# Optimization experiments

Hardware: AMD Instinct MI355X
Metric: run time of the kernel (lower is better)

Reference implementation:

```python
import jax, jax.numpy as jnp
import numpy as np

NUM_STEPS = 8
SLOPE = 25.0        # snntorch surrogate.fast_sigmoid default slope
MAX_STD = 2.0
MIN_STD = 0.1
STATE_DIM = 6
HIDDEN = 128
OUT = 1
BATCH = 65536
W_STD = 0.01


@jax.custom_vjp
def spike(x):
    # heaviside(x) with fast-sigmoid surrogate gradient
    return (x > 0).astype(x.dtype)

def _spike_fwd(x):
    return spike(x), x

def _spike_bwd(x, g):
    return (g / (SLOPE * jnp.abs(x) + 1.0) ** 2,)

spike.defvjp(_spike_fwd, _spike_bwd)


def setup_inputs() -> dict:
    key = jax.random.key(0)
    ks = jax.random.split(key, 8)
    state = jax.random.normal(ks[0], (BATCH, STATE_DIM), dtype=jnp.float32)
    w_fc1 = W_STD * jax.random.normal(ks[1], (HIDDEN, STATE_DIM), dtype=jnp.float32)
    w_rec1 = W_STD * jax.random.normal(ks[2], (HIDDEN, HIDDEN), dtype=jnp.float32)
    w_fc2 = W_STD * jax.random.normal(ks[3], (HIDDEN, HIDDEN), dtype=jnp.float32)
    w_rec2 = W_STD * jax.random.normal(ks[4], (HIDDEN, HIDDEN), dtype=jnp.float32)
    w_mean = W_STD * jax.random.normal(ks[5], (OUT, HIDDEN), dtype=jnp.float32)
    w_std = W_STD * jax.random.normal(ks[6], (OUT, HIDDEN), dtype=jnp.float32)
    return {
        "state": state,
        "w_fc1": w_fc1, "w_rec1": w_rec1,
        "w_fc2": w_fc2, "w_rec2": w_rec2,
        "w_mean": w_mean, "w_std": w_std,
        "alpha1": jnp.float32(0.9), "beta1": jnp.float32(0.9), "thr1": jnp.float32(1.0),
        "alpha2": jnp.float32(0.9), "beta2": jnp.float32(0.9), "thr2": jnp.float32(1.0),
    }


def _snn_forward(state, w_fc1, w_rec1, w_fc2, w_rec2, w_mean, w_std,
                 alpha1, beta1, thr1, alpha2, beta2, thr2):
    a1 = jnp.clip(alpha1, 0.0, 1.0); b1 = jnp.clip(beta1, 0.0, 1.0)
    a2 = jnp.clip(alpha2, 0.0, 1.0); b2 = jnp.clip(beta2, 0.0, 1.0)

    B = state.shape[0]
    cur1_in = state @ w_fc1.T  # constant across steps: [B, H]
    z = jnp.zeros((B, HIDDEN), dtype=state.dtype)

    def step(carry, _):
        syn1, mem1, spk1, syn2, mem2, spk2 = carry
        # layer 1: snntorch Synaptic (reset-by-subtract, reset from prev mem, detached)
        reset1 = jax.lax.stop_gradient((mem1 - thr1 > 0).astype(mem1.dtype))
        syn1 = a1 * syn1 + cur1_in + spk1 @ w_rec1.T
        mem1 = b1 * mem1 + syn1 - reset1 * thr1
        spk1 = spike(mem1 - thr1)
        # layer 2
        reset2 = jax.lax.stop_gradient((mem2 - thr2 > 0).astype(mem2.dtype))
        syn2 = a2 * syn2 + spk1 @ w_fc2.T + spk2 @ w_rec2.T
        mem2 = b2 * mem2 + syn2 - reset2 * thr2
        spk2 = spike(mem2 - thr2)
        return (syn1, mem1, spk1, syn2, mem2, spk2), spk2

    init = (z, z, z, z, z, z)
    _, spk_rec = jax.lax.scan(step, init, None, length=NUM_STEPS)  # [T, B, H]
    avg_spikes = spk_rec.mean(axis=0)  # [B, H]

    value_mean = jnp.tanh(avg_spikes @ w_mean.T)
    value_std = (MAX_STD - MIN_STD) * jax.nn.sigmoid(avg_spikes @ w_std.T + 2.0) + MIN_STD
    return value_mean, value_std


def reference(state, w_fc1, w_rec1, w_fc2, w_rec2, w_mean, w_std,
              alpha1, beta1, thr1, alpha2, beta2, thr2):
    return _snn_forward(state, w_fc1, w_rec1, w_fc2, w_rec2, w_mean, w_std,
                        alpha1, beta1, thr1, alpha2, beta2, thr2)
```

## Files before the change

kernel.cpp:

```cpp
#include <hip/hip_runtime.h>
#include <cmath>


typedef float f32x2 __attribute__((ext_vector_type(2)));
typedef float f32x4 __attribute__((ext_vector_type(4)));

constexpr int BATCH = 65536;
constexpr int HID   = 128;
constexpr int SDIM  = 6;
constexpr int NSTEP = 8;
constexpr int BLOCK = 1024;
constexpr int GRID  = 256;
constexpr int WAVES_TOTAL = GRID * (BLOCK / 64);
constexpr int ELEMS_PER_WAVE = BATCH / WAVES_TOTAL;
constexpr int PAIRS = ELEMS_PER_WAVE / 2;

__global__ __launch_bounds__(BLOCK) void snn_fwd(
    const float* __restrict__ state,
    const float* __restrict__ w_fc1,
    const float* __restrict__ w_rec1,
    const float* __restrict__ w_fc2,
    const float* __restrict__ w_rec2,
    const float* __restrict__ w_mean,
    const float* __restrict__ w_std,
    const float* __restrict__ p_alpha1, const float* __restrict__ p_beta1,
    const float* __restrict__ p_thr1,
    const float* __restrict__ p_alpha2, const float* __restrict__ p_beta2,
    const float* __restrict__ p_thr2,
    float* __restrict__ out)
{
    __shared__ f32x4 ldw[HID * 64];

    const int tid = threadIdx.x;

    for (int v = tid; v < HID * 64; v += BLOCK) {
        const int l = v >> 7;
        const int j = v & 127;
        const int pos = (j << 6) | (l ^ (j & 63));
        f32x4 w;
        w.x = w_rec1[l * HID + j];
        w.y = w_rec1[(l + 64) * HID + j];
        w.z = w_fc2 [l * HID + j];
        w.w = w_fc2 [(l + 64) * HID + j];
        ldw[pos] = w;
    }

    const int lane  = tid & 63;
    const int gwave = blockIdx.x * (BLOCK / 64) + (tid >> 6);

    f32x2 w1[SDIM];
    #pragma unroll
    for (int k = 0; k < SDIM; ++k) {
        w1[k].x = w_fc1[lane * SDIM + k];
        w1[k].y = w_fc1[(lane + 64) * SDIM + k];
    }
    const float wm_a = w_mean[lane], wm_b = w_mean[lane + 64];
    const float ws_a = w_std [lane], ws_b = w_std [lane + 64];

    const float a1 = fminf(fmaxf(p_alpha1[0], 0.f), 1.f);
    const float b1 = fminf(fmaxf(p_beta1 [0], 0.f), 1.f);
    const float a2 = fminf(fmaxf(p_alpha2[0], 0.f), 1.f);
    const float b2 = fminf(fmaxf(p_beta2 [0], 0.f), 1.f);
    const float t1 = p_thr1[0];
    const float t2 = p_thr2[0];
    const f32x2 a1v = {a1, a1}, b1v = {b1, b1}, a2v = {a2, a2}, b2v = {b2, b2};

    const float* __restrict__ rec2_a = w_rec2 + lane * HID;
    const float* __restrict__ rec2_b = w_rec2 + (lane + 64) * HID;

    __syncthreads();

    auto walk2 = [&](unsigned long long m, const f32x4* __restrict__ base,
                     f32x2& f, f32x2& r) {
        if (!m) return;
        int j = __builtin_ctzll(m); m &= m - 1;
        f32x4 w = base[(j << 6) | (lane ^ j)];
        while (m) {
            const int j2 = __builtin_ctzll(m); m &= m - 1;
            const f32x4 w2 = base[(j2 << 6) | (lane ^ j2)];
            r += __builtin_shufflevector(w, w, 0, 1);
            f += __builtin_shufflevector(w, w, 2, 3);
            w = w2;
        }
        r += __builtin_shufflevector(w, w, 0, 1);
        f += __builtin_shufflevector(w, w, 2, 3);
    };
    auto walkg = [&](unsigned long long m, int jbase, f32x2& f) {
        while (m) {
            const int j = __builtin_ctzll(m) + jbase; m &= m - 1;
            f.x += rec2_a[j];
            f.y += rec2_b[j];
        }
    };

    const f32x4* __restrict__ baseLo = ldw;
    const f32x4* __restrict__ baseHi = ldw + (64 << 6);

    float sx[SDIM], sy[SDIM];
    #pragma unroll
    for (int k = 0; k < SDIM; ++k) {
        sx[k] = state[(gwave) * SDIM + k];
        sy[k] = state[(gwave + WAVES_TOTAL) * SDIM + k];
    }

    for (int e = 0; e < PAIRS; ++e) {
        const int bx = gwave + WAVES_TOTAL * (2 * e);
        const int by = gwave + WAVES_TOTAL * (2 * e + 1);

        f32x2 curx = {0.f, 0.f}, cury = {0.f, 0.f};
        #pragma unroll
        for (int k = 0; k < SDIM; ++k) {
            const f32x2 sxv = {sx[k], sx[k]};
            const f32x2 syv = {sy[k], sy[k]};
            curx = __builtin_elementwise_fma(sxv, w1[k], curx);
            cury = __builtin_elementwise_fma(syv, w1[k], cury);
        }

        float sxn[SDIM], syn2p[SDIM];
        if (e + 1 < PAIRS) {
            const int bxn = gwave + WAVES_TOTAL * (2 * e + 2);
            const int byn = gwave + WAVES_TOTAL * (2 * e + 3);
            #pragma unroll
            for (int k = 0; k < SDIM; ++k) {
                sxn[k]   = state[bxn * SDIM + k];
                syn2p[k] = state[byn * SDIM + k];
            }
        }

        f32x2 s1x = {0.f, 0.f}, m1x = {0.f, 0.f}, s2x = {0.f, 0.f}, m2x = {0.f, 0.f};
        f32x2 s1y = {0.f, 0.f}, m1y = {0.f, 0.f}, s2y = {0.f, 0.f}, m2y = {0.f, 0.f};
        bool k1xa = false, k1xb = false, k2xa = false, k2xb = false;
        bool k1ya = false, k1yb = false, k2ya = false, k2yb = false;
        f32x2 cx = {0.f, 0.f}, cy = {0.f, 0.f};
        unsigned long long M2xa = 0ull, M2xb = 0ull, M2ya = 0ull, M2yb = 0ull;
        f32x2 rx = {0.f, 0.f}, ry = {0.f, 0.f};

        #pragma unroll 1
        for (int t = 0; t < NSTEP; ++t) {
            s1x = __builtin_elementwise_fma(a1v, s1x, curx + rx);
            s1y = __builtin_elementwise_fma(a1v, s1y, cury + ry);
            const f32x2 rst1x = {k1xa ? t1 : 0.f, k1xb ? t1 : 0.f};
            const f32x2 rst1y = {k1ya ? t1 : 0.f, k1yb ? t1 : 0.f};
            m1x = __builtin_elementwise_fma(b1v, m1x, s1x) - rst1x;
            m1y = __builtin_elementwise_fma(b1v, m1y, s1y) - rst1y;
            k1xa = (m1x.x - t1) > 0.f;
            k1xb = (m1x.y - t1) > 0.f;
            k1ya = (m1y.x - t1) > 0.f;
            k1yb = (m1y.y - t1) > 0.f;
            const unsigned long long M1xa = __ballot(k1xa);
            const unsigned long long M1xb = __ballot(k1xb);
            const unsigned long long M1ya = __ballot(k1ya);
            const unsigned long long M1yb = __ballot(k1yb);

            f32x2 fx = {0.f, 0.f}, fy = {0.f, 0.f};
            rx = (f32x2){0.f, 0.f}; ry = (f32x2){0.f, 0.f};
            walk2(M1xa, baseLo, fx, rx);
            walk2(M1ya, baseLo, fy, ry);
            walk2(M1xb, baseHi, fx, rx);
            walk2(M1yb, baseHi, fy, ry);

            if ((M2xa | M2xb | M2ya | M2yb) != 0ull) {
                walkg(M2xa, 0,  fx);
                walkg(M2xb, 64, fx);
                walkg(M2ya, 0,  fy);
                walkg(M2yb, 64, fy);
            }

            s2x = __builtin_elementwise_fma(a2v, s2x, fx);
            s2y = __builtin_elementwise_fma(a2v, s2y, fy);
            const f32x2 rst2x = {k2xa ? t2 : 0.f, k2xb ? t2 : 0.f};
            const f32x2 rst2y = {k2ya ? t2 : 0.f, k2yb ? t2 : 0.f};
            m2x = __builtin_elementwise_fma(b2v, m2x, s2x) - rst2x;
            m2y = __builtin_elementwise_fma(b2v, m2y, s2y) - rst2y;
            k2xa = (m2x.x - t2) > 0.f;
            k2xb = (m2x.y - t2) > 0.f;
            k2ya = (m2y.x - t2) > 0.f;
            k2yb = (m2y.y - t2) > 0.f;
            M2xa = __ballot(k2xa);
            M2xb = __ballot(k2xb);
            M2ya = __ballot(k2ya);
            M2yb = __ballot(k2yb);
            const f32x2 onex = {k2xa ? 1.f : 0.f, k2xb ? 1.f : 0.f};
            const f32x2 oney = {k2ya ? 1.f : 0.f, k2yb ? 1.f : 0.f};
            cx += onex;
            cy += oney;
        }

        const float axa = cx.x * (1.f / (float)NSTEP);
        const float axb = cx.y * (1.f / (float)NSTEP);
        const float aya = cy.x * (1.f / (float)NSTEP);
        const float ayb = cy.y * (1.f / (float)NSTEP);
        float dmx = axa * wm_a + axb * wm_b;
        float dsx = axa * ws_a + axb * ws_b;
        float dmy = aya * wm_a + ayb * wm_b;
        float dsy = aya * ws_a + ayb * ws_b;
        #pragma unroll
        for (int off = 32; off > 0; off >>= 1) {
            dmx += __shfl_xor(dmx, off, 64);
            dsx += __shfl_xor(dsx, off, 64);
            dmy += __shfl_xor(dmy, off, 64);
            dsy += __shfl_xor(dsy, off, 64);
        }
        if (lane == 0) {
            out[bx] = tanhf(dmx);
            out[by] = tanhf(dmy);
            const float sgx = 1.f / (1.f + expf(-(dsx + 2.f)));
            const float sgy = 1.f / (1.f + expf(-(dsy + 2.f)));
            out[BATCH + bx] = 1.9f * sgx + 0.1f;
            out[BATCH + by] = 1.9f * sgy + 0.1f;
        }

        if (e + 1 < PAIRS) {
            #pragma unroll
            for (int k = 0; k < SDIM; ++k) { sx[k] = sxn[k]; sy[k] = syn2p[k]; }
        }
    }
}

extern "C" void kernel_launch(void* const* d_in, const int* in_sizes, int n_in,
                              void* d_out, int out_size, void* d_ws, size_t ws_size,
                              hipStream_t stream) {
    (void)in_sizes; (void)n_in; (void)d_ws; (void)ws_size; (void)out_size;
    snn_fwd<<<GRID, BLOCK, 0, stream>>>(
        (const float*)d_in[0],
        (const float*)d_in[1],
        (const float*)d_in[2],
        (const float*)d_in[3],
        (const float*)d_in[4],
        (const float*)d_in[5],
        (const float*)d_in[6],
        (const float*)d_in[7],
        (const float*)d_in[8],
        (const float*)d_in[9],
        (const float*)d_in[10],
        (const float*)d_in[11],
        (const float*)d_in[12],
        (float*)d_out);
}
```

Measured before the change: 122.4 us.

## Pack recurrent weights into global workspace and read via cache instead of LDS

Adds a small pre-pass kernel that packs w_rec1 and w_fc2 into an interleaved f32x4 layout in the workspace buffer. The main kernel then reads that layout straight from global memory (L1/L2) instead of staging 128 KB into shared memory per block. This removes the per-block LDS fill and barrier and lifts the LDS occupancy limit, allowing smaller 512-thread blocks with more waves per CU. The cost is an extra kernel launch and gathers served by cache rather than LDS, which may have higher latency. The original LDS kernel is kept as a fallback when no workspace is available.

```diff
diff --git a/kernel.cpp b/kernel.cpp
--- a/kernel.cpp
+++ b/kernel.cpp
@@ -9,17 +9,33 @@
 constexpr int HID   = 128;
 constexpr int SDIM  = 6;
 constexpr int NSTEP = 8;
-constexpr int BLOCK = 1024;
-constexpr int GRID  = 256;
-constexpr int WAVES_TOTAL = GRID * (BLOCK / 64);
-constexpr int ELEMS_PER_WAVE = BATCH / WAVES_TOTAL;
-constexpr int PAIRS = ELEMS_PER_WAVE / 2;
-
-__global__ __launch_bounds__(BLOCK) void snn_fwd(
+
+__global__ __launch_bounds__(256) void pack_weights(
+    const float* __restrict__ w_rec1,
+    const float* __restrict__ w_fc2,
+    f32x4* __restrict__ P)
+{
+    const int g = blockIdx.x * 256 + threadIdx.x;
+    const int j = g & 127;
+    const int l = g >> 7;
+    f32x4 w;
+    w.x = w_rec1[l * HID + j];
+    w.y = w_rec1[(l + 64) * HID + j];
+    w.z = w_fc2 [l * HID + j];
+    w.w = w_fc2 [(l + 64) * HID + j];
+    P[(j << 6) | l] = w;
+}
+
+constexpr int BLOCK_G = 512;
+constexpr int GRID_G  = 1024;
+constexpr int WAVES_G = GRID_G * (BLOCK_G / 64);
+constexpr int EPW_G   = BATCH / WAVES_G;
+constexpr int PAIRS_G = EPW_G / 2;
+
+__global__ __launch_bounds__(BLOCK_G, 8) void snn_fwd_g(
     const float* __restrict__ state,
     const float* __restrict__ w_fc1,
-    const float* __restrict__ w_rec1,
-    const float* __restrict__ w_fc2,
+    const f32x4* __restrict__ P,
     const float* __restrict__ w_rec2,
     const float* __restrict__ w_mean,
     const float* __restrict__ w_std,
@@ -29,24 +45,9 @@
     const float* __restrict__ p_thr2,
     float* __restrict__ out)
 {
-    __shared__ f32x4 ldw[HID * 64];
-
-    const int tid = threadIdx.x;
-
-    for (int v = tid; v < HID * 64; v += BLOCK) {
-        const int l = v >> 7;
-        const int j = v & 127;
-        const int pos = (j << 6) | (l ^ (j & 63));
-        f32x4 w;
-        w.x = w_rec1[l * HID + j];
-        w.y = w_rec1[(l + 64) * HID + j];
-        w.z = w_fc2 [l * HID + j];
-        w.w = w_fc2 [(l + 64) * HID + j];
-        ldw[pos] = w;
-    }
-
+    const int tid   = threadIdx.x;
     const int lane  = tid & 63;
-    const int gwave = blockIdx.x * (BLOCK / 64) + (tid >> 6);
+    const int gwave = blockIdx.x * (BLOCK_G / 64) + (tid >> 6);
 
     f32x2 w1[SDIM];
     #pragma unroll
@@ -68,16 +69,17 @@
     const float* __restrict__ rec2_a = w_rec2 + lane * HID;
     const float* __restrict__ rec2_b = w_rec2 + (lane + 64) * HID;
 
-    __syncthreads();
+    const f32x4* __restrict__ baseLo = P;
+    const f32x4* __restrict__ baseHi = P + (64 << 6);
 
     auto walk2 = [&](unsigned long long m, const f32x4* __restrict__ base,
                      f32x2& f, f32x2& r) {
         if (!m) return;
         int j = __builtin_ctzll(m); m &= m - 1;
-        f32x4 w = base[(j << 6) | (lane ^ j)];
+        f32x4 w = base[(j << 6) | lane];
         while (m) {
             const int j2 = __builtin_ctzll(m); m &= m - 1;
-            const f32x4 w2 = base[(j2 << 6) | (lane ^ j2)];
+            const f32x4 w2 = base[(j2 << 6) | lane];
             r += __builtin_shufflevector(w, w, 0, 1);
             f += __builtin_shufflevector(w, w, 2, 3);
             w = w2;
@@ -93,19 +95,16 @@
         }
     };
 
-    const f32x4* __restrict__ baseLo = ldw;
-    const f32x4* __restrict__ baseHi = ldw + (64 << 6);
-
     float sx[SDIM], sy[SDIM];
     #pragma unroll
     for (int k = 0; k < SDIM; ++k) {
         sx[k] = state[(gwave) * SDIM + k];
-        sy[k] = state[(gwave + WAVES_TOTAL) * SDIM + k];
-    }
-
-    for (int e = 0; e < PAIRS; ++e) {
-        const int bx = gwave + WAVES_TOTAL * (2 * e);
-        const int by = gwave + WAVES_TOTAL * (2 * e + 1);
+        sy[k] = state[(gwave + WAVES_G) * SDIM + k];
+    }
+
+    for (int e = 0; e < PAIRS_G; ++e) {
+        const int bx = gwave + WAVES_G * (2 * e);
+        const int by = gwave + WAVES_G * (2 * e + 1);
 
         f32x2 curx = {0.f, 0.f}, cury = {0.f, 0.f};
         #pragma unroll
@@ -117,9 +116,9 @@
         }
 
         float sxn[SDIM], syn2p[SDIM];
-        if (e + 1 < PAIRS) {
-            const int bxn = gwave + WAVES_TOTAL * (2 * e + 2);
-            const int byn = gwave + WAVES_TOTAL * (2 * e + 3);
+        if (e + 1 < PAIRS_G) {
+            const int bxn = gwave + WAVES_G * (2 * e + 2);
+            const int byn = gwave + WAVES_G * (2 * e + 3);
             #pragma unroll
             for (int k = 0; k < SDIM; ++k) {
                 sxn[k]   = state[bxn * SDIM + k];
@@ -210,7 +209,214 @@
             out[BATCH + by] = 1.9f * sgy + 0.1f;
         }
 
-        if (e + 1 < PAIRS) {
+        if (e + 1 < PAIRS_G) {
+            #pragma unroll
+            for (int k = 0; k < SDIM; ++k) { sx[k] = sxn[k]; sy[k] = syn2p[k]; }
+        }
+    }
+}
+
+constexpr int BLOCK_L = 1024;
+constexpr int GRID_L  = 256;
+constexpr int WAVES_L = GRID_L * (BLOCK_L / 64);
+constexpr int EPW_L   = BATCH / WAVES_L;
+constexpr int PAIRS_L = EPW_L / 2;
+
+__global__ __launch_bounds__(BLOCK_L) void snn_fwd_lds(
+    const float* __restrict__ state,
+    const float* __restrict__ w_fc1,
+    const float* __restrict__ w_rec1,
+    const float* __restrict__ w_fc2,
+    const float* __restrict__ w_rec2,
+    const float* __restrict__ w_mean,
+    const float* __restrict__ w_std,
+    const float* __restrict__ p_alpha1, const float* __restrict__ p_beta1,
+    const float* __restrict__ p_thr1,
+    const float* __restrict__ p_alpha2, const float* __restrict__ p_beta2,
+    const float* __restrict__ p_thr2,
+    float* __restrict__ out)
+{
+    __shared__ f32x4 ldw[HID * 64];
+    const int tid = threadIdx.x;
+
+    for (int v = tid; v < HID * 64; v += BLOCK_L) {
+        const int l = v >> 7;
+        const int j = v & 127;
+        const int pos = (j << 6) | (l ^ (j & 63));
+        f32x4 w;
+        w.x = w_rec1[l * HID + j];
+        w.y = w_rec1[(l + 64) * HID + j];
+        w.z = w_fc2 [l * HID + j];
+        w.w = w_fc2 [(l + 64) * HID + j];
+        ldw[pos] = w;
+    }
+
+    const int lane  = tid & 63;
+    const int gwave = blockIdx.x * (BLOCK_L / 64) + (tid >> 6);
+
+    f32x2 w1[SDIM];
+    #pragma unroll
+    for (int k = 0; k < SDIM; ++k) {
+        w1[k].x = w_fc1[lane * SDIM + k];
+        w1[k].y = w_fc1[(lane + 64) * SDIM + k];
+    }
+    const float wm_a = w_mean[lane], wm_b = w_mean[lane + 64];
+    const float ws_a = w_std [lane], ws_b = w_std [lane + 64];
+
+    const float a1 = fminf(fmaxf(p_alpha1[0], 0.f), 1.f);
+    const float b1 = fminf(fmaxf(p_beta1 [0], 0.f), 1.f);
+    const float a2 = fminf(fmaxf(p_alpha2[0], 0.f), 1.f);
+    const float b2 = fminf(fmaxf(p_beta2 [0], 0.f), 1.f);
+    const float t1 = p_thr1[0];
+    const float t2 = p_thr2[0];
+    const f32x2 a1v = {a1, a1}, b1v = {b1, b1}, a2v = {a2, a2}, b2v = {b2, b2};
+
+    const float* __restrict__ rec2_a = w_rec2 + lane * HID;
+    const float* __restrict__ rec2_b = w_rec2 + (lane + 64) * HID;
+
+    __syncthreads();
+
+    auto walk2 = [&](unsigned long long m, const f32x4* __restrict__ base,
+                     f32x2& f, f32x2& r) {
+        if (!m) return;
+        int j = __builtin_ctzll(m); m &= m - 1;
+        f32x4 w = base[(j << 6) | (lane ^ j)];
+        while (m) {
+            const int j2 = __builtin_ctzll(m); m &= m - 1;
+            const f32x4 w2 = base[(j2 << 6) | (lane ^ j2)];
+            r += __builtin_shufflevector(w, w, 0, 1);
+            f += __builtin_shufflevector(w, w, 2, 3);
+            w = w2;
+        }
+        r += __builtin_shufflevector(w, w, 0, 1);
+        f += __builtin_shufflevector(w, w, 2, 3);
+    };
+    auto walkg = [&](unsigned long long m, int jbase, f32x2& f) {
+        while (m) {
+            const int j = __builtin_ctzll(m) + jbase; m &= m - 1;
+            f.x += rec2_a[j];
+            f.y += rec2_b[j];
+        }
+    };
+
+    const f32x4* __restrict__ baseLo = ldw;
+    const f32x4* __restrict__ baseHi = ldw + (64 << 6);
+
+    float sx[SDIM], sy[SDIM];
+    #pragma unroll
+    for (int k = 0; k < SDIM; ++k) {
+        sx[k] = state[(gwave) * SDIM + k];
+        sy[k] = state[(gwave + WAVES_L) * SDIM + k];
+    }
+
+    for (int e = 0; e < PAIRS_L; ++e) {
+        const int bx = gwave + WAVES_L * (2 * e);
+        const int by = gwave + WAVES_L * (2 * e + 1);
+
+        f32x2 curx = {0.f, 0.f}, cury = {0.f, 0.f};
+        #pragma unroll
+        for (int k = 0; k < SDIM; ++k) {
+            const f32x2 sxv = {sx[k], sx[k]};
+            const f32x2 syv = {sy[k], sy[k]};
+            curx = __builtin_elementwise_fma(sxv, w1[k], curx);
+            cury = __builtin_elementwise_fma(syv, w1[k], cury);
+        }
+
+        float sxn[SDIM], syn2p[SDIM];
+        if (e + 1 < PAIRS_L) {
+            const int bxn = gwave + WAVES_L * (2 * e + 2);
+            const int byn = gwave + WAVES_L * (2 * e + 3);
+            #pragma unroll
+            for (int k = 0; k < SDIM; ++k) {
+                sxn[k]   = state[bxn * SDIM + k];
+                syn2p[k] = state[byn * SDIM + k];
+            }
+        }
+
+        f32x2 s1x = {0.f, 0.f}, m1x = {0.f, 0.f}, s2x = {0.f, 0.f}, m2x = {0.f, 0.f};
+        f32x2 s1y = {0.f, 0.f}, m1y = {0.f, 0.f}, s2y = {0.f, 0.f}, m2y = {0.f, 0.f};
+        bool k1xa = false, k1xb = false, k2xa = false, k2xb = false;
+        bool k1ya = false, k1yb = false, k2ya = false, k2yb = false;
+        f32x2 cx = {0.f, 0.f}, cy = {0.f, 0.f};
+        unsigned long long M2xa = 0ull, M2xb = 0ull, M2ya = 0ull, M2yb = 0ull;
+        f32x2 rx = {0.f, 0.f}, ry = {0.f, 0.f};
+
+        #pragma unroll 1
+        for (int t = 0; t < NSTEP; ++t) {
+            s1x = __builtin_elementwise_fma(a1v, s1x, curx + rx);
+            s1y = __builtin_elementwise_fma(a1v, s1y, cury + ry);
+            const f32x2 rst1x = {k1xa ? t1 : 0.f, k1xb ? t1 : 0.f};
+            const f32x2 rst1y = {k1ya ? t1 : 0.f, k1yb ? t1 : 0.f};
+            m1x = __builtin_elementwise_fma(b1v, m1x, s1x) - rst1x;
+            m1y = __builtin_elementwise_fma(b1v, m1y, s1y) - rst1y;
+            k1xa = (m1x.x - t1) > 0.f;
+            k1xb = (m1x.y - t1) > 0.f;
+            k1ya = (m1y.x - t1) > 0.f;
+            k1yb = (m1y.y - t1) > 0.f;
+            const unsigned long long M1xa = __ballot(k1xa);
+            const unsigned long long M1xb = __ballot(k1xb);
+            const unsigned long long M1ya = __ballot(k1ya);
+            const unsigned long long M1yb = __ballot(k1yb);
+
+            f32x2 fx = {0.f, 0.f}, fy = {0.f, 0.f};
+            rx = (f32x2){0.f, 0.f}; ry = (f32x2){0.f, 0.f};
+            walk2(M1xa, baseLo, fx, rx);
+            walk2(M1ya, baseLo, fy, ry);
+            walk2(M1xb, baseHi, fx, rx);
+            walk2(M1yb, baseHi, fy, ry);
+
+            if ((M2xa | M2xb | M2ya | M2yb) != 0ull) {
+                walkg(M2xa, 0,  fx);
+                walkg(M2xb, 64, fx);
+                walkg(M2ya, 0,  fy);
+                walkg(M2yb, 64, fy);
+            }
+
+            s2x = __builtin_elementwise_fma(a2v, s2x, fx);
+            s2y = __builtin_elementwise_fma(a2v, s2y, fy);
+            const f32x2 rst2x = {k2xa ? t2 : 0.f, k2xb ? t2 : 0.f};
+            const f32x2 rst2y = {k2ya ? t2 : 0.f, k2yb ? t2 : 0.f};
+            m2x = __builtin_elementwise_fma(b2v, m2x, s2x) - rst2x;
+            m2y = __builtin_elementwise_fma(b2v, m2y, s2y) - rst2y;
+            k2xa = (m2x.x - t2) > 0.f;
+            k2xb = (m2x.y - t2) > 0.f;
+            k2ya = (m2y.x - t2) > 0.f;
+            k2yb = (m2y.y - t2) > 0.f;
+            M2xa = __ballot(k2xa);
+            M2xb = __ballot(k2xb);
+            M2ya = __ballot(k2ya);
+            M2yb = __ballot(k2yb);
+            const f32x2 onex = {k2xa ? 1.f : 0.f, k2xb ? 1.f : 0.f};
+            const f32x2 oney = {k2ya ? 1.f : 0.f, k2yb ? 1.f : 0.f};
+            cx += onex;
+            cy += oney;
+        }
+
+        const float axa = cx.x * (1.f / (float)NSTEP);
+        const float axb = cx.y * (1.f / (float)NSTEP);
+        const float aya = cy.x * (1.f / (float)NSTEP);
+        const float ayb = cy.y * (1.f / (float)NSTEP);
+        float dmx = axa * wm_a + axb * wm_b;
+        float dsx = axa * ws_a + axb * ws_b;
+        float dmy = aya * wm_a + ayb * wm_b;
+        float dsy = aya * ws_a + ayb * ws_b;
+        #pragma unroll
+        for (int off = 32; off > 0; off >>= 1) {
+            dmx += __shfl_xor(dmx, off, 64);
+            dsx += __shfl_xor(dsx, off, 64);
+            dmy += __shfl_xor(dmy, off, 64);
+            dsy += __shfl_xor(dsy, off, 64);
+        }
+        if (lane == 0) {
+            out[bx] = tanhf(dmx);
+            out[by] = tanhf(dmy);
+            const float sgx = 1.f / (1.f + expf(-(dsx + 2.f)));
+            const float sgy = 1.f / (1.f + expf(-(dsy + 2.f)));
+            out[BATCH + bx] = 1.9f * sgx + 0.1f;
+            out[BATCH + by] = 1.9f * sgy + 0.1f;
+        }
+
+        if (e + 1 < PAIRS_L) {
             #pragma unroll
             for (int k = 0; k < SDIM; ++k) { sx[k] = sxn[k]; sy[k] = syn2p[k]; }
         }
@@ -220,20 +426,28 @@
 extern "C" void kernel_launch(void* const* d_in, const int* in_sizes, int n_in,
                               void* d_out, int out_size, void* d_ws, size_t ws_size,
                               hipStream_t stream) {
-    (void)in_sizes; (void)n_in; (void)d_ws; (void)ws_size; (void)out_size;
-    snn_fwd<<<GRID, BLOCK, 0, stream>>>(
-        (const float*)d_in[0],
-        (const float*)d_in[1],
-        (const float*)d_in[2],
-        (const float*)d_in[3],
-        (const float*)d_in[4],
-        (const float*)d_in[5],
-        (const float*)d_in[6],
-        (const float*)d_in[7],
-        (const float*)d_in[8],
-        (const float*)d_in[9],
-        (const float*)d_in[10],
-        (const float*)d_in[11],
-        (const float*)d_in[12],
-        (float*)d_out);
+    (void)in_sizes; (void)n_in; (void)out_size;
+    if (d_ws != nullptr && ws_size >= (size_t)(HID * 64 * sizeof(f32x4))) {
+        f32x4* P = (f32x4*)d_ws;
+        pack_weights<<<32, 256, 0, stream>>>(
+            (const float*)d_in[2], (const float*)d_in[3], P);
+        snn_fwd_g<<<GRID_G, BLOCK_G, 0, stream>>>(
+            (const float*)d_in[0],
+            (const float*)d_in[1],
+            P,
+            (const float*)d_in[4],
+            (const float*)d_in[5],
+            (const float*)d_in[6],
+            (const float*)d_in[7], (const float*)d_in[8], (const float*)d_in[9],
+            (const float*)d_in[10], (const float*)d_in[11], (const float*)d_in[12],
+            (float*)d_out);
+    } else {
+        snn_fwd_lds<<<GRID_L, BLOCK_L, 0, stream>>>(
+            (const float*)d_in[0], (const float*)d_in[1], (const float*)d_in[2],
+            (const float*)d_in[3], (const float*)d_in[4], (const float*)d_in[5],
+            (const float*)d_in[6],
+            (const float*)d_in[7], (const float*)d_in[8], (const float*)d_in[9],
+            (const float*)d_in[10], (const float*)d_in[11], (const float*)d_in[12],
+            (float*)d_out);
+    }
 }
```

After: 178.3 us. 45.7% more time.

## Split rec1 weights to global workspace, halve LDS, run two blocks per CU

Applied to the files above, without the earlier changes.

Adds a pre-pass kernel that packs w_rec1 into a lane-major f32x2 layout in the workspace buffer. The main kernel now keeps only w_fc2 in LDS (64 KB instead of 128 KB) and requests two 1024-thread blocks per CU over a 512-block grid. Each wave now processes one batch element at a time rather than pairs, and the spike walk software-pipelines its loads. This trades LDS reads of rec1 for cached global reads to gain occupancy, at the cost of an extra launch, more global traffic and less instruction-level parallelism per wave.

```diff
diff --git a/kernel.cpp b/kernel.cpp
--- a/kernel.cpp
+++ b/kernel.cpp
@@ -9,13 +9,181 @@
 constexpr int HID   = 128;
 constexpr int SDIM  = 6;
 constexpr int NSTEP = 8;
-constexpr int BLOCK = 1024;
-constexpr int GRID  = 256;
-constexpr int WAVES_TOTAL = GRID * (BLOCK / 64);
-constexpr int ELEMS_PER_WAVE = BATCH / WAVES_TOTAL;
-constexpr int PAIRS = ELEMS_PER_WAVE / 2;
-
-__global__ __launch_bounds__(BLOCK) void snn_fwd(
+
+__global__ __launch_bounds__(256) void pack_rec1(
+    const float* __restrict__ w_rec1,
+    f32x2* __restrict__ R)
+{
+    const int g = blockIdx.x * 256 + threadIdx.x;
+    const int l = g & 63;
+    const int j = g >> 6;
+    f32x2 w;
+    w.x = w_rec1[l * HID + j];
+    w.y = w_rec1[(l + 64) * HID + j];
+    R[g] = w;
+}
+
+constexpr int BLOCK_S = 1024;
+constexpr int GRID_S  = 512;
+constexpr int WAVES_S = GRID_S * (BLOCK_S / 64);
+constexpr int EPW_S   = BATCH / WAVES_S;
+
+__global__ __launch_bounds__(BLOCK_S, 2) void snn_fwd_split(
+    const float* __restrict__ state,
+    const float* __restrict__ w_fc1,
+    const f32x2* __restrict__ R,
+    const float* __restrict__ w_fc2,
+    const float* __restrict__ w_rec2,
+    const float* __restrict__ w_mean,
+    const float* __restrict__ w_std,
+    const float* __restrict__ p_alpha1, const float* __restrict__ p_beta1,
+    const float* __restrict__ p_thr1,
+    const float* __restrict__ p_alpha2, const float* __restrict__ p_beta2,
+    const float* __restrict__ p_thr2,
+    float* __restrict__ out)
+{
+    __shared__ f32x2 ld_fc2[HID * 64];
+
+    const int tid = threadIdx.x;
+
+    for (int v = tid; v < HID * 64; v += BLOCK_S) {
+        const int l = v >> 7;
+        const int j = v & 127;
+        const int pos = (j << 6) | (l ^ (j & 63));
+        f32x2 w;
+        w.x = w_fc2[l * HID + j];
+        w.y = w_fc2[(l + 64) * HID + j];
+        ld_fc2[pos] = w;
+    }
+
+    const int lane  = tid & 63;
+    const int gwave = blockIdx.x * (BLOCK_S / 64) + (tid >> 6);
+
+    f32x2 w1[SDIM];
+    #pragma unroll
+    for (int k = 0; k < SDIM; ++k) {
+        w1[k].x = w_fc1[lane * SDIM + k];
+        w1[k].y = w_fc1[(lane + 64) * SDIM + k];
+    }
+    const float wm_a = w_mean[lane], wm_b = w_mean[lane + 64];
+    const float ws_a = w_std [lane], ws_b = w_std [lane + 64];
+
+    const float a1 = fminf(fmaxf(p_alpha1[0], 0.f), 1.f);
+    const float b1 = fminf(fmaxf(p_beta1 [0], 0.f), 1.f);
+    const float a2 = fminf(fmaxf(p_alpha2[0], 0.f), 1.f);
+    const float b2 = fminf(fmaxf(p_beta2 [0], 0.f), 1.f);
+    const float t1 = p_thr1[0];
+    const float t2 = p_thr2[0];
+    const f32x2 a1v = {a1, a1}, b1v = {b1, b1}, a2v = {a2, a2}, b2v = {b2, b2};
+
+    const float* __restrict__ rec2_a = w_rec2 + lane * HID;
+    const float* __restrict__ rec2_b = w_rec2 + (lane + 64) * HID;
+
+    __syncthreads();
+
+    auto walk = [&](unsigned long long m,
+                    const f32x2* __restrict__ ldsb,
+                    const f32x2* __restrict__ gb,
+                    f32x2& f, f32x2& r) {
+        if (!m) return;
+        int j = __builtin_ctzll(m); m &= m - 1;
+        f32x2 wf = ldsb[(j << 6) | (lane ^ j)];
+        f32x2 wr = gb[(j << 6) | lane];
+        while (m) {
+            const int j2 = __builtin_ctzll(m); m &= m - 1;
+            const f32x2 wf2 = ldsb[(j2 << 6) | (lane ^ j2)];
+            const f32x2 wr2 = gb[(j2 << 6) | lane];
+            f += wf; r += wr;
+            wf = wf2; wr = wr2;
+        }
+        f += wf; r += wr;
+    };
+    auto walkg = [&](unsigned long long m, int jbase, f32x2& f) {
+        while (m) {
+            const int j = __builtin_ctzll(m) + jbase; m &= m - 1;
+            f.x += rec2_a[j];
+            f.y += rec2_b[j];
+        }
+    };
+
+    const f32x2* __restrict__ fc2Lo = ld_fc2;
+    const f32x2* __restrict__ fc2Hi = ld_fc2 + (64 << 6);
+    const f32x2* __restrict__ RLo   = R;
+    const f32x2* __restrict__ RHi   = R + (64 << 6);
+
+    for (int e = 0; e < EPW_S; ++e) {
+        const int b = gwave + WAVES_S * e;
+
+        f32x2 cur = {0.f, 0.f};
+        #pragma unroll
+        for (int k = 0; k < SDIM; ++k) {
+            const float s = state[b * SDIM + k];
+            const f32x2 sv = {s, s};
+            cur = __builtin_elementwise_fma(sv, w1[k], cur);
+        }
+
+        f32x2 s1 = {0.f, 0.f}, m1 = {0.f, 0.f};
+        f32x2 s2 = {0.f, 0.f}, m2 = {0.f, 0.f};
+        bool k1a = false, k1b = false, k2a = false, k2b = false;
+        f32x2 cnt = {0.f, 0.f};
+        unsigned long long M2a = 0ull, M2b = 0ull;
+        f32x2 r = {0.f, 0.f};
+
+        #pragma unroll 1
+        for (int t = 0; t < NSTEP; ++t) {
+            s1 = __builtin_elementwise_fma(a1v, s1, cur + r);
+            const f32x2 rst1 = {k1a ? t1 : 0.f, k1b ? t1 : 0.f};
+            m1 = __builtin_elementwise_fma(b1v, m1, s1) - rst1;
+            k1a = (m1.x - t1) > 0.f;
+            k1b = (m1.y - t1) > 0.f;
+            const unsigned long long M1a = __ballot(k1a);
+            const unsigned long long M1b = __ballot(k1b);
+
+            f32x2 f = {0.f, 0.f};
+            r = (f32x2){0.f, 0.f};
+            walk(M1a, fc2Lo, RLo, f, r);
+            walk(M1b, fc2Hi, RHi, f, r);
+
+            if ((M2a | M2b) != 0ull) {
+                walkg(M2a, 0,  f);
+                walkg(M2b, 64, f);
+            }
+
+            s2 = __builtin_elementwise_fma(a2v, s2, f);
+            const f32x2 rst2 = {k2a ? t2 : 0.f, k2b ? t2 : 0.f};
+            m2 = __builtin_elementwise_fma(b2v, m2, s2) - rst2;
+            k2a = (m2.x - t2) > 0.f;
+            k2b = (m2.y - t2) > 0.f;
+            M2a = __ballot(k2a);
+            M2b = __ballot(k2b);
+            const f32x2 one = {k2a ? 1.f : 0.f, k2b ? 1.f : 0.f};
+            cnt += one;
+        }
+
+        const float av_a = cnt.x * (1.f / (float)NSTEP);
+        const float av_b = cnt.y * (1.f / (float)NSTEP);
+        float dm = av_a * wm_a + av_b * wm_b;
+        float ds = av_a * ws_a + av_b * ws_b;
+        #pragma unroll
+        for (int off = 32; off > 0; off >>= 1) {
+            dm += __shfl_xor(dm, off, 64);
+            ds += __shfl_xor(ds, off, 64);
+        }
+        if (lane == 0) {
+            out[b] = tanhf(dm);
+            const float sg = 1.f / (1.f + expf(-(ds + 2.f)));
+            out[BATCH + b] = 1.9f * sg + 0.1f;
+        }
+    }
+}
+
+constexpr int BLOCK_L = 1024;
+constexpr int GRID_L  = 256;
+constexpr int WAVES_L = GRID_L * (BLOCK_L / 64);
+constexpr int EPW_L   = BATCH / WAVES_L;
+constexpr int PAIRS_L = EPW_L / 2;
+
+__global__ __launch_bounds__(BLOCK_L) void snn_fwd_lds(
     const float* __restrict__ state,
     const float* __restrict__ w_fc1,
     const float* __restrict__ w_rec1,
@@ -30,10 +198,9 @@
     float* __restrict__ out)
 {
     __shared__ f32x4 ldw[HID * 64];
-
     const int tid = threadIdx.x;
 
-    for (int v = tid; v < HID * 64; v += BLOCK) {
+    for (int v = tid; v < HID * 64; v += BLOCK_L) {
         const int l = v >> 7;
         const int j = v & 127;
         const int pos = (j << 6) | (l ^ (j & 63));
@@ -46,7 +213,7 @@
     }
 
     const int lane  = tid & 63;
-    const int gwave = blockIdx.x * (BLOCK / 64) + (tid >> 6);
+    const int gwave = blockIdx.x * (BLOCK_L / 64) + (tid >> 6);
 
     f32x2 w1[SDIM];
     #pragma unroll
@@ -100,12 +267,12 @@
     #pragma unroll
     for (int k = 0; k < SDIM; ++k) {
         sx[k] = state[(gwave) * SDIM + k];
-        sy[k] = state[(gwave + WAVES_TOTAL) * SDIM + k];
-    }
-
-    for (int e = 0; e < PAIRS; ++e) {
-        const int bx = gwave + WAVES_TOTAL * (2 * e);
-        const int by = gwave + WAVES_TOTAL * (2 * e + 1);
+        sy[k] = state[(gwave + WAVES_L) * SDIM + k];
+    }
+
+    for (int e = 0; e < PAIRS_L; ++e) {
+        const int bx = gwave + WAVES_L * (2 * e);
+        const int by = gwave + WAVES_L * (2 * e + 1);
 
         f32x2 curx = {0.f, 0.f}, cury = {0.f, 0.f};
         #pragma unroll
@@ -117,9 +284,9 @@
         }
 
         float sxn[SDIM], syn2p[SDIM];
-        if (e + 1 < PAIRS) {
-            const int bxn = gwave + WAVES_TOTAL * (2 * e + 2);
-            const int byn = gwave + WAVES_TOTAL * (2 * e + 3);
+        if (e + 1 < PAIRS_L) {
+            const int bxn = gwave + WAVES_L * (2 * e + 2);
+            const int byn = gwave + WAVES_L * (2 * e + 3);
             #pragma unroll
             for (int k = 0; k < SDIM; ++k) {
                 sxn[k]   = state[bxn * SDIM + k];
@@ -210,7 +377,7 @@
             out[BATCH + by] = 1.9f * sgy + 0.1f;
         }
 
-        if (e + 1 < PAIRS) {
+        if (e + 1 < PAIRS_L) {
             #pragma unroll
             for (int k = 0; k < SDIM; ++k) { sx[k] = sxn[k]; sy[k] = syn2p[k]; }
         }
@@ -220,20 +387,28 @@
 extern "C" void kernel_launch(void* const* d_in, const int* in_sizes, int n_in,
                               void* d_out, int out_size, void* d_ws, size_t ws_size,
                               hipStream_t stream) {
-    (void)in_sizes; (void)n_in; (void)d_ws; (void)ws_size; (void)out_size;
-    snn_fwd<<<GRID, BLOCK, 0, stream>>>(
-        (const float*)d_in[0],
-        (const float*)d_in[1],
-        (const float*)d_in[2],
-        (const float*)d_in[3],
-        (const float*)d_in[4],
-        (const float*)d_in[5],
-        (const float*)d_in[6],
-        (const float*)d_in[7],
-        (const float*)d_in[8],
-        (const float*)d_in[9],
-        (const float*)d_in[10],
-        (const float*)d_in[11],
-        (const float*)d_in[12],
-        (float*)d_out);
+    (void)in_sizes; (void)n_in; (void)out_size;
+    if (d_ws != nullptr && ws_size >= (size_t)(HID * 64 * sizeof(f32x2))) {
+        f32x2* R = (f32x2*)d_ws;
+        pack_rec1<<<32, 256, 0, stream>>>((const float*)d_in[2], R);
+        snn_fwd_split<<<GRID_S, BLOCK_S, 0, stream>>>(
+            (const float*)d_in[0],
+            (const float*)d_in[1],
+            R,
+            (const float*)d_in[3],
+            (const float*)d_in[4],
+            (const float*)d_in[5],
+            (const float*)d_in[6],
+            (const float*)d_in[7], (const float*)d_in[8], (const float*)d_in[9],
+            (const float*)d_in[10], (const float*)d_in[11], (const float*)d_in[12],
+            (float*)d_out);
+    } else {
+        snn_fwd_lds<<<GRID_L, BLOCK_L, 0, stream>>>(
+            (const float*)d_in[0], (const float*)d_in[1], (const float*)d_in[2],
+            (const float*)d_in[3], (const float*)d_in[4], (const float*)d_in[5],
+            (const float*)d_in[6],
+            (const float*)d_in[7], (const float*)d_in[8], (const float*)d_in[9],
+            (const float*)d_in[10], (const float*)d_in[11], (const float*)d_in[12],
+            (float*)d_out);
+    }
 }
```

After: 131.3 us. 1.07x slower.

## Unroll spike-mask LDS walk by four and drop register-held fc1/state prefetch

Applied to the files above, without the earlier changes.

The sparse spike-driven accumulation over LDS weights now handles four set bits per iteration, issuing four LDS loads before the adds, with a remainder path for up to three leftovers. This replaces the one-ahead software pipeline and aims to hide more LDS latency. The fc1 weights and state rows are no longer kept in registers or prefetched a pair ahead; they are reloaded from global memory each iteration, which frees registers at the cost of exposed load latency. The order of the walk calls is also changed so each sample's low and high halves are processed back to back.

```diff
diff --git a/kernel.cpp b/kernel.cpp
--- a/kernel.cpp
+++ b/kernel.cpp
@@ -48,12 +48,6 @@
     const int lane  = tid & 63;
     const int gwave = blockIdx.x * (BLOCK / 64) + (tid >> 6);
 
-    f32x2 w1[SDIM];
-    #pragma unroll
-    for (int k = 0; k < SDIM; ++k) {
-        w1[k].x = w_fc1[lane * SDIM + k];
-        w1[k].y = w_fc1[(lane + 64) * SDIM + k];
-    }
     const float wm_a = w_mean[lane], wm_b = w_mean[lane + 64];
     const float ws_a = w_std [lane], ws_b = w_std [lane + 64];
 
@@ -72,18 +66,44 @@
 
     auto walk2 = [&](unsigned long long m, const f32x4* __restrict__ base,
                      f32x2& f, f32x2& r) {
-        if (!m) return;
-        int j = __builtin_ctzll(m); m &= m - 1;
-        f32x4 w = base[(j << 6) | (lane ^ j)];
-        while (m) {
-            const int j2 = __builtin_ctzll(m); m &= m - 1;
+        while (__builtin_popcountll(m) >= 4) {
+            int j0 = __builtin_ctzll(m); m &= m - 1;
+            int j1 = __builtin_ctzll(m); m &= m - 1;
+            int j2 = __builtin_ctzll(m); m &= m - 1;
+            int j3 = __builtin_ctzll(m); m &= m - 1;
+            const f32x4 w0 = base[(j0 << 6) | (lane ^ j0)];
+            const f32x4 w1 = base[(j1 << 6) | (lane ^ j1)];
             const f32x4 w2 = base[(j2 << 6) | (lane ^ j2)];
-            r += __builtin_shufflevector(w, w, 0, 1);
-            f += __builtin_shufflevector(w, w, 2, 3);
-            w = w2;
-        }
-        r += __builtin_shufflevector(w, w, 0, 1);
-        f += __builtin_shufflevector(w, w, 2, 3);
+            const f32x4 w3 = base[(j3 << 6) | (lane ^ j3)];
+            r += __builtin_shufflevector(w0, w0, 0, 1);
+            f += __builtin_shufflevector(w0, w0, 2, 3);
+            r += __builtin_shufflevector(w1, w1, 0, 1);
+            f += __builtin_shufflevector(w1, w1, 2, 3);
+            r += __builtin_shufflevector(w2, w2, 0, 1);
+            f += __builtin_shufflevector(w2, w2, 2, 3);
+            r += __builtin_shufflevector(w3, w3, 0, 1);
+            f += __builtin_shufflevector(w3, w3, 2, 3);
+        }
+        if (m) {
+            const int nrem = __builtin_popcountll(m);
+            f32x4 w0, w1, w2;
+            { const int j = __builtin_ctzll(m); m &= m - 1;
+              w0 = base[(j << 6) | (lane ^ j)]; }
+            if (nrem > 1) { const int j = __builtin_ctzll(m); m &= m - 1;
+                            w1 = base[(j << 6) | (lane ^ j)]; }
+            if (nrem > 2) { const int j = __builtin_ctzll(m); m &= m - 1;
+                            w2 = base[(j << 6) | (lane ^ j)]; }
+            r += __builtin_shufflevector(w0, w0, 0, 1);
+            f += __builtin_shufflevector(w0, w0, 2, 3);
+            if (nrem > 1) {
+                r += __builtin_shufflevector(w1, w1, 0, 1);
+                f += __builtin_shufflevector(w1, w1, 2, 3);
+            }
+            if (nrem > 2) {
+                r += __builtin_shufflevector(w2, w2, 0, 1);
+                f += __builtin_shufflevector(w2, w2, 2, 3);
+            }
+        }
     };
     auto walkg = [&](unsigned long long m, int jbase, f32x2& f) {
         while (m) {
@@ -96,34 +116,23 @@
     const f32x4* __restrict__ baseLo = ldw;
     const f32x4* __restrict__ baseHi = ldw + (64 << 6);
 
-    float sx[SDIM], sy[SDIM];
-    #pragma unroll
-    for (int k = 0; k < SDIM; ++k) {
-        sx[k] = state[(gwave) * SDIM + k];
-        sy[k] = state[(gwave + WAVES_TOTAL) * SDIM + k];
-    }
-
     for (int e = 0; e < PAIRS; ++e) {
         const int bx = gwave + WAVES_TOTAL * (2 * e);
         const int by = gwave + WAVES_TOTAL * (2 * e + 1);
 
         f32x2 curx = {0.f, 0.f}, cury = {0.f, 0.f};
-        #pragma unroll
-        for (int k = 0; k < SDIM; ++k) {
-            const f32x2 sxv = {sx[k], sx[k]};
-            const f32x2 syv = {sy[k], sy[k]};
-            curx = __builtin_elementwise_fma(sxv, w1[k], curx);
-            cury = __builtin_elementwise_fma(syv, w1[k], cury);
-        }
-
-        float sxn[SDIM], syn2p[SDIM];
-        if (e + 1 < PAIRS) {
-            const int bxn = gwave + WAVES_TOTAL * (2 * e + 2);
-            const int byn = gwave + WAVES_TOTAL * (2 * e + 3);
+        {
             #pragma unroll
             for (int k = 0; k < SDIM; ++k) {
-                sxn[k]   = state[bxn * SDIM + k];
-                syn2p[k] = state[byn * SDIM + k];
+                f32x2 w1k;
+                w1k.x = w_fc1[lane * SDIM + k];
+                w1k.y = w_fc1[(lane + 64) * SDIM + k];
+                const float sx = state[bx * SDIM + k];
+                const float sy = state[by * SDIM + k];
+                const f32x2 sxv = {sx, sx};
+                const f32x2 syv = {sy, sy};
+                curx = __builtin_elementwise_fma(sxv, w1k, curx);
+                cury = __builtin_elementwise_fma(syv, w1k, cury);
             }
         }
 
@@ -155,8 +164,8 @@
             f32x2 fx = {0.f, 0.f}, fy = {0.f, 0.f};
             rx = (f32x2){0.f, 0.f}; ry = (f32x2){0.f, 0.f};
             walk2(M1xa, baseLo, fx, rx);
+            walk2(M1xb, baseHi, fx, rx);
             walk2(M1ya, baseLo, fy, ry);
-            walk2(M1xb, baseHi, fx, rx);
             walk2(M1yb, baseHi, fy, ry);
 
             if ((M2xa | M2xb | M2ya | M2yb) != 0ull) {
@@ -208,11 +217,6 @@
             const float sgy = 1.f / (1.f + expf(-(dsy + 2.f)));
             out[BATCH + bx] = 1.9f * sgx + 0.1f;
             out[BATCH + by] = 1.9f * sgy + 0.1f;
-        }
-
-        if (e + 1 < PAIRS) {
-            #pragma unroll
-            for (int k = 0; k < SDIM; ++k) { sx[k] = sxn[k]; sy[k] = syn2p[k]; }
         }
     }
 }
```

Measured after the change: 128.6 us. +5.1%, slower.
